# Kernel tuning notes

Measured on AMD Instinct MI355X. Metric: run time of the kernel, lower is better.

## Reference

```python
import jax, jax.numpy as jnp
import numpy as np

# e2m1 FP4 value table: sign bit in nibble MSB, values {0,0.5,1,1.5,2,3,4,6}
_E2M1 = jnp.array([0.0, 0.5, 1.0, 1.5, 2.0, 3.0, 4.0, 6.0,
                   -0.0, -0.5, -1.0, -1.5, -2.0, -3.0, -4.0, -6.0], dtype=jnp.float32)


def _dequant_fp4(packed, scales, group_size):
    """packed: [E, out, in//8] uint32; scales: [E, in//group_size, out] -> [E, out, in] f32."""
    shifts = jnp.arange(8, dtype=jnp.uint32) * 4  # nibble shift amounts 0,4,...,28
    nib = (packed[..., None] >> shifts) & jnp.uint32(0xF)  # [E, out, in//8, 8]
    E, O, P, _ = nib.shape
    nib = nib.reshape(E, O, P * 8).astype(jnp.int32)
    w = _E2M1[nib]  # [E, out, in] f32
    gids = jnp.arange(P * 8) // group_size  # group id per input column
    sc = jnp.transpose(scales, (0, 2, 1))[:, :, gids]  # [E, out, in]
    return w * sc


def setup_inputs() -> dict:
    E, H, I, T, K, G = 8, 2048, 1408, 2048, 2, 128
    key = jax.random.key(0)
    ks = jax.random.split(key, 9)
    x = jax.random.normal(ks[0], (T, H), dtype=jnp.float32)
    gate_packed = jax.random.bits(ks[1], (E, I, H // 8), dtype=jnp.uint32)
    up_packed = jax.random.bits(ks[2], (E, I, H // 8), dtype=jnp.uint32)
    down_packed = jax.random.bits(ks[3], (E, H, I // 8), dtype=jnp.uint32)
    gate_scales = jax.random.uniform(ks[4], (E, H // G, I), jnp.float32, 0.5, 1.5)
    up_scales = jax.random.uniform(ks[5], (E, H // G, I), jnp.float32, 0.5, 1.5)
    down_scales = jax.random.uniform(ks[6], (E, I // G, H), jnp.float32, 0.5, 1.5)
    topk_idx = jax.random.randint(ks[7], (T, K), 0, E, dtype=jnp.int32)
    w = jax.random.uniform(ks[8], (T, K), jnp.float32)
    topk_w = w / jnp.sum(w, axis=-1, keepdims=True)
    return {"x": x,
            "gate_packed": gate_packed, "gate_scales": gate_scales,
            "up_packed": up_packed, "up_scales": up_scales,
            "down_packed": down_packed, "down_scales": down_scales,
            "topk_idx": topk_idx, "topk_w": topk_w, "group_size": G}


def reference(x, gate_packed, gate_scales, up_packed, up_scales,
              down_packed, down_scales, topk_idx, topk_w, group_size):
    # Fused dequant (nibble unpack + e2m1 table + per-group scale) for all experts
    gate_w = _dequant_fp4(gate_packed, gate_scales, group_size)  # [E, I, H]
    up_w = _dequant_fp4(up_packed, up_scales, group_size)        # [E, I, H]
    down_w = _dequant_fp4(down_packed, down_scales, group_size)  # [E, H, I]
    # Grouped SwiGLU expert MLP (dense over E=8 experts, gather routed outputs)
    g = jnp.einsum('th,eih->eti', x, gate_w)
    u = jnp.einsum('th,eih->eti', x, up_w)
    h = jax.nn.silu(g) * u                                        # [E, T, I]
    y = jnp.einsum('eti,ehi->eth', h, down_w)                     # [E, T, H]
    T = x.shape[0]
    sel = y[topk_idx, jnp.arange(T)[:, None], :]                  # [T, K, H]
    return jnp.sum(sel * topk_w[..., None], axis=1)               # [T, H]
```

## Files before the change

### kernel.cpp

```cpp
#include <hip/hip_runtime.h>
#include <hip/hip_bf16.h>
#include <stdint.h>

#define E_ 8
#define H_ 2048
#define I_ 1408
#define T_ 2048
#define K_ 2
#define G_ 128

typedef __bf16 bf16;
typedef bf16 bf16x8 __attribute__((ext_vector_type(8)));
typedef float f32x4 __attribute__((ext_vector_type(4)));

__device__ __forceinline__ uint32_t prm(uint32_t hi, uint32_t lo, uint32_t sel) {
    return __builtin_amdgcn_perm(hi, lo, sel);
}

struct DequantTab { uint32_t thi0, thi1, tlo0, tlo1; };

__device__ __forceinline__ DequantTab build_tab(float s) {
    union { bf16 h[8]; uint32_t u[4]; } tb;
    tb.h[0] = (bf16)(0.0f);
    tb.h[1] = (bf16)(0.5f * s);
    tb.h[2] = (bf16)(1.0f * s);
    tb.h[3] = (bf16)(1.5f * s);
    tb.h[4] = (bf16)(2.0f * s);
    tb.h[5] = (bf16)(3.0f * s);
    tb.h[6] = (bf16)(4.0f * s);
    tb.h[7] = (bf16)(6.0f * s);
    DequantTab t;
    t.thi0 = prm(tb.u[1], tb.u[0], 0x07050301u);
    t.tlo0 = prm(tb.u[1], tb.u[0], 0x06040200u);
    t.thi1 = prm(tb.u[3], tb.u[2], 0x07050301u);
    t.tlo1 = prm(tb.u[3], tb.u[2], 0x06040200u);
    return t;
}

__device__ __forceinline__ uint4 dequant8t(uint32_t p, const DequantTab& t) {
    const uint32_t pr = p >> 4;
    const uint32_t pe = p  & 0x07070707u;
    const uint32_t po = pr & 0x07070707u;
    const uint32_t He = prm(t.thi1, t.thi0, pe) | ((p  & 0x08080808u) << 4);
    const uint32_t Le = prm(t.tlo1, t.tlo0, pe);
    const uint32_t Ho = prm(t.thi1, t.thi0, po) | ((pr & 0x08080808u) << 4);
    const uint32_t Lo = prm(t.tlo1, t.tlo0, po);
    const uint32_t E01 = prm(He, Le, 0x05010400u);
    const uint32_t E23 = prm(He, Le, 0x07030602u);
    const uint32_t O01 = prm(Ho, Lo, 0x05010400u);
    const uint32_t O23 = prm(Ho, Lo, 0x07030602u);
    return make_uint4(prm(O01, E01, 0x05040100u),
                      prm(O01, E01, 0x07060302u),
                      prm(O23, E23, 0x05040100u),
                      prm(O23, E23, 0x07060302u));
}

__device__ __forceinline__ void gld16(void* lds, const void* g) {
    __builtin_amdgcn_global_load_lds(
        (__attribute__((address_space(1))) void*)g,
        (__attribute__((address_space(3))) void*)lds, 16, 0, 0);
}

#define SB0() __builtin_amdgcn_sched_barrier(0)

#define DQW(WD, PW, TAB) do { \
    uint4 d0_ = dequant8t((PW).x, (TAB)); \
    uint4 d1_ = dequant8t((PW).y, (TAB)); \
    uint4 d2_ = dequant8t((PW).z, (TAB)); \
    uint4 d3_ = dequant8t((PW).w, (TAB)); \
    *(uint4*)&WD[wrow][((cb + 0) ^ rs) * 8] = d0_; \
    *(uint4*)&WD[wrow][((cb + 1) ^ rs) * 8] = d1_; \
    *(uint4*)&WD[wrow][((cb + 2) ^ rs) * 8] = d2_; \
    *(uint4*)&WD[wrow][((cb + 3) ^ rs) * 8] = d3_; \
} while (0)

__global__ void route_count(const int* __restrict__ topk_idx, int* __restrict__ counts) {
    int p = blockIdx.x * blockDim.x + threadIdx.x;
    if (p < T_ * K_) atomicAdd(&counts[topk_idx[p]], 1);
}

__global__ void route_scan(const int* __restrict__ counts, int* __restrict__ offsets,
                           int* __restrict__ tmap) {
    if (threadIdx.x == 0) {
        int acc = 0, ti = 0;
        for (int e = 0; e < E_; e++) {
            offsets[e] = acc;
            int nt = (counts[e] + 127) >> 7;
            for (int j = 0; j < nt; j++) tmap[ti++] = (e << 16) | j;
            acc += counts[e];
        }
        offsets[E_] = acc;
        for (; ti < 64; ti++) tmap[ti] = -1;
    }
}

__global__ void route_fill(const int* __restrict__ topk_idx, const float* __restrict__ topk_w,
                           int* __restrict__ cursors, const int* __restrict__ offsets,
                           int* __restrict__ tok, float* __restrict__ wgt,
                           int* __restrict__ inv) {
    int p = blockIdx.x * blockDim.x + threadIdx.x;
    if (p < T_ * K_) {
        int e = topk_idx[p];
        int slot = atomicAdd(&cursors[e], 1);
        int idx = offsets[e] + slot;
        tok[idx] = p / K_;
        wgt[idx] = topk_w[p];
        inv[p] = idx;
    }
}

__global__ __launch_bounds__(256)
void xcast_kernel(const float* __restrict__ x, uint4* __restrict__ xb) {
    const int i = blockIdx.x * 256 + threadIdx.x;
    const float4 a = ((const float4*)x)[i * 2];
    const float4 b = ((const float4*)x)[i * 2 + 1];
    union { uint4 u; bf16 h[8]; } r;
    r.h[0] = (bf16)a.x; r.h[1] = (bf16)a.y; r.h[2] = (bf16)a.z; r.h[3] = (bf16)a.w;
    r.h[4] = (bf16)b.x; r.h[5] = (bf16)b.y; r.h[6] = (bf16)b.z; r.h[7] = (bf16)b.w;
    xb[i] = r.u;
}

__global__ __launch_bounds__(256, 2)
void gemm1t_kernel(const bf16* __restrict__ xb,
                   const uint32_t* __restrict__ gate_packed,
                   const float* __restrict__ gate_scales,
                   const uint32_t* __restrict__ up_packed,
                   const float* __restrict__ up_scales,
                   const int* __restrict__ offsets,
                   const int* __restrict__ tmap,
                   const int* __restrict__ tok, bf16* __restrict__ h_buf)
{
    const int tm = tmap[blockIdx.x];
    if (tm < 0) return;
    const int e = tm >> 16, ty = tm & 0xffff;
    const int row0 = offsets[e];
    const int cnt = offsets[e + 1] - row0;
    const int itile = blockIdx.y;

    __shared__ __align__(16) bf16 xs0[128][64];
    __shared__ __align__(16) bf16 xs1[128][64];
    __shared__ __align__(16) bf16 wgs0[64][64];
    __shared__ __align__(16) bf16 wgs1[64][64];
    __shared__ __align__(16) bf16 wus0[64][64];
    __shared__ __align__(16) bf16 wus1[64][64];

    const int tid = threadIdx.x;

    const int xr = tid >> 3;
    const int xc = tid & 7;
    const int xch = (xc ^ (xr & 7)) * 8;
    const bf16* xsrc[4];
    bf16 *xdst0[4], *xdst1[4];
#pragma unroll
    for (int j = 0; j < 4; ++j) {
        int g = ty * 128 + xr + j * 32;
        g = (g < cnt) ? g : (cnt - 1);
        xsrc[j] = xb + (size_t)tok[row0 + g] * H_ + xch;
        xdst0[j] = &xs0[xr + j * 32][xc * 8];
        xdst1[j] = &xs1[xr + j * 32][xc * 8];
    }

    const int mat  = tid >> 7;
    const int id   = tid & 127;
    const int wrow = id >> 1;
    const int quad = id & 1;
    const int cb = quad * 4, rs = wrow & 7;
    const int irow = itile * 64 + wrow;
    const uint32_t* wp_row = (mat ? up_packed : gate_packed)
        + (size_t)e * I_ * (H_ / 8) + (size_t)irow * (H_ / 8) + quad * 4;
    const float* ws_row = (mat ? up_scales : gate_scales)
        + (size_t)e * (H_ / G_) * I_ + irow;
    bf16 (* const wd0)[64] = mat ? wus0 : wgs0;
    bf16 (* const wd1)[64] = mat ? wus1 : wgs1;

    const int wave = tid >> 6, lane = tid & 63;
    const int wy = wave >> 1, wx = wave & 1;
    const int lrow = lane & 15, kq = lane >> 4;

    f32x4 accg[4][2] = {};
    f32x4 accu[4][2] = {};

    constexpr int NG = H_ / G_;

#define MFMA1(XS, WG, WU) do { \
    _Pragma("unroll") \
    for (int kh = 0; kh < 2; ++kh) { \
        bf16x8 a[4], bg[2], bu[2]; \
        _Pragma("unroll") \
        for (int mi = 0; mi < 4; ++mi) { \
            const int ra = wy * 64 + mi * 16 + lrow; \
            a[mi] = *(const bf16x8*)&XS[ra][((kh * 4 + kq) ^ (ra & 7)) * 8]; \
        } \
        _Pragma("unroll") \
        for (int ni = 0; ni < 2; ++ni) { \
            const int rbq = wx * 32 + ni * 16 + lrow; \
            const int cbq = ((kh * 4 + kq) ^ (rbq & 7)) * 8; \
            bg[ni] = *(const bf16x8*)&WG[rbq][cbq]; \
            bu[ni] = *(const bf16x8*)&WU[rbq][cbq]; \
        } \
        _Pragma("unroll") \
        for (int mi = 0; mi < 4; ++mi) \
            _Pragma("unroll") \
            for (int ni = 0; ni < 2; ++ni) { \
                accg[mi][ni] = __builtin_amdgcn_mfma_f32_16x16x32_bf16(a[mi], bg[ni], accg[mi][ni], 0, 0, 0); \
                accu[mi][ni] = __builtin_amdgcn_mfma_f32_16x16x32_bf16(a[mi], bu[ni], accu[mi][ni], 0, 0, 0); \
            } \
    } \
} while (0)

#pragma unroll
    for (int j = 0; j < 4; ++j) gld16(xdst0[j], xsrc[j]);
    SB0();
    uint4 pw0 = *(const uint4*)(wp_row);
    uint4 pwO = *(const uint4*)(wp_row + 8);
    float sc0 = ws_row[0];
    SB0();
    DequantTab tab = build_tab(sc0);
    DQW(wd0, pw0, tab);
    asm volatile("s_waitcnt lgkmcnt(0)" ::: "memory");
    __builtin_amdgcn_s_barrier();
    SB0();

    float scn = 0.f;
    uint4 pwE;
    for (int kg = 0; kg < NG; ++kg) {
        const bool last = (kg == NG - 1);
#pragma unroll
        for (int j = 0; j < 4; ++j) gld16(xdst1[j], xsrc[j] + (kg * 2 + 1) * 64);
        SB0();
        if (!last) {
            pwE = *(const uint4*)(wp_row + (size_t)(kg * 2 + 2) * 8);
            scn = ws_row[(size_t)(kg + 1) * I_];
        }
        SB0();
        DQW(wd1, pwO, tab);
        MFMA1(xs0, wgs0, wus0);
        SB0();
        if (!last) asm volatile("s_waitcnt vmcnt(2) lgkmcnt(0)" ::: "memory");
        else       asm volatile("s_waitcnt vmcnt(0) lgkmcnt(0)" ::: "memory");
        __builtin_amdgcn_s_barrier();
        SB0();

        if (!last) {
#pragma unroll
            for (int j = 0; j < 4; ++j) gld16(xdst0[j], xsrc[j] + (kg * 2 + 2) * 64);
            SB0();
            pwO = *(const uint4*)(wp_row + (size_t)(kg * 2 + 3) * 8);
            SB0();
            tab = build_tab(scn);
            DQW(wd0, pwE, tab);
            MFMA1(xs1, wgs1, wus1);
            SB0();
            asm volatile("s_waitcnt vmcnt(1) lgkmcnt(0)" ::: "memory");
            __builtin_amdgcn_s_barrier();
            SB0();
        } else {
            MFMA1(xs1, wgs1, wus1);
            SB0();
            asm volatile("s_waitcnt lgkmcnt(0)" ::: "memory");
            __builtin_amdgcn_s_barrier();
            SB0();
        }
    }

#pragma unroll
    for (int mi = 0; mi < 4; ++mi)
#pragma unroll
        for (int ni = 0; ni < 2; ++ni) {
            const int icol = itile * 64 + wx * 32 + ni * 16 + lrow;
#pragma unroll
            for (int r = 0; r < 4; ++r) {
                const int grow = ty * 128 + wy * 64 + mi * 16 + kq * 4 + r;
                if (grow < cnt) {
                    const float gv = accg[mi][ni][r];
                    const float hv = gv / (1.f + __expf(-gv)) * accu[mi][ni][r];
                    h_buf[(size_t)(row0 + grow) * I_ + icol] = (bf16)hv;
                }
            }
        }
#undef MFMA1
}

__global__ __launch_bounds__(256, 2)
void gemm2t_kernel(const bf16* __restrict__ h_buf,
                   const uint32_t* __restrict__ down_packed,
                   const float* __restrict__ down_scales,
                   const int* __restrict__ offsets,
                   const int* __restrict__ tmap,
                   const float* __restrict__ wgt, float* __restrict__ yp)
{
    const int tm = tmap[blockIdx.x];
    if (tm < 0) return;
    const int e = tm >> 16, ty = tm & 0xffff;
    const int row0 = offsets[e];
    const int cnt = offsets[e + 1] - row0;
    const int htile = blockIdx.y;

    __shared__ __align__(16) bf16 hs0[128][64];
    __shared__ __align__(16) bf16 hs1[128][64];
    __shared__ __align__(16) bf16 wds0[128][64];
    __shared__ __align__(16) bf16 wds1[128][64];

    const int tid = threadIdx.x;

    const int xr = tid >> 3;
    const int xc = tid & 7;
    const int xch = (xc ^ (xr & 7)) * 8;
    const bf16* hsrc[4];
    bf16 *hdst0[4], *hdst1[4];
#pragma unroll
    for (int j = 0; j < 4; ++j) {
        int g = ty * 128 + xr + j * 32;
        g = (g < cnt) ? g : (cnt - 1);
        hsrc[j] = h_buf + (size_t)(row0 + g) * I_ + xch;
        hdst0[j] = &hs0[xr + j * 32][xc * 8];
        hdst1[j] = &hs1[xr + j * 32][xc * 8];
    }

    const int wrow = tid >> 1;
    const int quad = tid & 1;
    const int cb = quad * 4, rs = wrow & 7;
    const int hrow = htile * 128 + wrow;
    const uint32_t* dp_row = down_packed + (size_t)e * H_ * (I_ / 8) + (size_t)hrow * (I_ / 8) + quad * 4;
    const float* ds_row = down_scales + (size_t)e * (I_ / G_) * H_ + hrow;

    const int wave = tid >> 6, lane = tid & 63;
    const int wy = wave >> 1, wx = wave & 1;
    const int lrow = lane & 15, kq = lane >> 4;

    f32x4 acc[4][4] = {};

    constexpr int NG = I_ / G_;

#define MFMA2(HS, WD) do { \
    _Pragma("unroll") \
    for (int kh = 0; kh < 2; ++kh) { \
        bf16x8 a[4], b[4]; \
        _Pragma("unroll") \
        for (int mi = 0; mi < 4; ++mi) { \
            const int ra = wy * 64 + mi * 16 + lrow; \
            a[mi] = *(const bf16x8*)&HS[ra][((kh * 4 + kq) ^ (ra & 7)) * 8]; \
        } \
        _Pragma("unroll") \
        for (int ni = 0; ni < 4; ++ni) { \
            const int rbq = wx * 64 + ni * 16 + lrow; \
            b[ni] = *(const bf16x8*)&WD[rbq][((kh * 4 + kq) ^ (rbq & 7)) * 8]; \
        } \
        _Pragma("unroll") \
        for (int mi = 0; mi < 4; ++mi) \
            _Pragma("unroll") \
            for (int ni = 0; ni < 4; ++ni) \
                acc[mi][ni] = __builtin_amdgcn_mfma_f32_16x16x32_bf16(a[mi], b[ni], acc[mi][ni], 0, 0, 0); \
    } \
} while (0)

#pragma unroll
    for (int j = 0; j < 4; ++j) gld16(hdst0[j], hsrc[j]);
    SB0();
    uint4 pw0 = *(const uint4*)(dp_row);
    uint4 pwO = *(const uint4*)(dp_row + 8);
    float sc0 = ds_row[0];
    SB0();
    DequantTab tab = build_tab(sc0);
    DQW(wds0, pw0, tab);
    asm volatile("s_waitcnt lgkmcnt(0)" ::: "memory");
    __builtin_amdgcn_s_barrier();
    SB0();

    float scn = 0.f;
    uint4 pwE;
    for (int kg = 0; kg < NG; ++kg) {
        const bool last = (kg == NG - 1);
#pragma unroll
        for (int j = 0; j < 4; ++j) gld16(hdst1[j], hsrc[j] + (kg * 2 + 1) * 64);
        SB0();
        if (!last) {
            pwE = *(const uint4*)(dp_row + (size_t)(kg * 2 + 2) * 8);
            scn = ds_row[(size_t)(kg + 1) * H_];
        }
        SB0();
        DQW(wds1, pwO, tab);
        MFMA2(hs0, wds0);
        SB0();
        if (!last) asm volatile("s_waitcnt vmcnt(2) lgkmcnt(0)" ::: "memory");
        else       asm volatile("s_waitcnt vmcnt(0) lgkmcnt(0)" ::: "memory");
        __builtin_amdgcn_s_barrier();
        SB0();

        if (!last) {
#pragma unroll
            for (int j = 0; j < 4; ++j) gld16(hdst0[j], hsrc[j] + (kg * 2 + 2) * 64);
            SB0();
            pwO = *(const uint4*)(dp_row + (size_t)(kg * 2 + 3) * 8);
            SB0();
            tab = build_tab(scn);
            DQW(wds0, pwE, tab);
            MFMA2(hs1, wds1);
            SB0();
            asm volatile("s_waitcnt vmcnt(1) lgkmcnt(0)" ::: "memory");
            __builtin_amdgcn_s_barrier();
            SB0();
        } else {
            MFMA2(hs1, wds1);
            SB0();
            asm volatile("s_waitcnt lgkmcnt(0)" ::: "memory");
            __builtin_amdgcn_s_barrier();
            SB0();
        }
    }

#pragma unroll
    for (int mi = 0; mi < 4; ++mi)
#pragma unroll
        for (int r = 0; r < 4; ++r) {
            const int lr = wy * 64 + mi * 16 + kq * 4 + r;
            const int grow = ty * 128 + lr;
            if (grow < cnt) {
                const float w = wgt[row0 + grow];
#pragma unroll
                for (int ni = 0; ni < 4; ++ni) {
                    const int col = htile * 128 + wx * 64 + ni * 16 + lrow;
                    yp[(size_t)(row0 + grow) * H_ + col] = acc[mi][ni][r] * w;
                }
            }
        }
#undef MFMA2
}

__global__ __launch_bounds__(256)
void combine_kernel(const float* __restrict__ yp, const int* __restrict__ inv,
                    float* __restrict__ out) {
    const int idx = blockIdx.x * 256 + threadIdx.x;
    const int t = idx >> 9;
    const int c = idx & 511;
    const float4 a = ((const float4*)yp)[(size_t)inv[t * 2] * (H_ / 4) + c];
    const float4 b = ((const float4*)yp)[(size_t)inv[t * 2 + 1] * (H_ / 4) + c];
    float4 o;
    o.x = a.x + b.x; o.y = a.y + b.y; o.z = a.z + b.z; o.w = a.w + b.w;
    ((float4*)out)[idx] = o;
}

extern "C" void kernel_launch(void* const* d_in, const int* in_sizes, int n_in,
                              void* d_out, int out_size, void* d_ws, size_t ws_size,
                              hipStream_t stream) {
    const float* x = (const float*)d_in[0];
    const uint32_t* gate_packed = (const uint32_t*)d_in[1];
    const float* gate_scales = (const float*)d_in[2];
    const uint32_t* up_packed = (const uint32_t*)d_in[3];
    const float* up_scales = (const float*)d_in[4];
    const uint32_t* down_packed = (const uint32_t*)d_in[5];
    const float* down_scales = (const float*)d_in[6];
    const int* topk_idx = (const int*)d_in[7];
    const float* topk_w = (const float*)d_in[8];
    float* out = (float*)d_out;

    char* ws = (char*)d_ws;
    int* counts  = (int*)ws;
    int* cursors = (int*)(ws + 32);
    int* offsets = (int*)(ws + 64);
    int* tmap    = (int*)(ws + 128);
    int* tok     = (int*)(ws + 640);
    float* wgt   = (float*)(ws + 17024);
    int* inv     = (int*)(ws + 33408);
    bf16* h_buf  = (bf16*)(ws + 49792);
    bf16* xb     = (bf16*)(ws + 49792 + 11534336ull);
    float* yp    = (float*)(ws + 49792 + 11534336ull + 8388608ull);

    hipMemsetAsync(d_ws, 0, 1024, stream);

    route_count<<<(T_ * K_ + 255) / 256, 256, 0, stream>>>(topk_idx, counts);
    route_scan<<<1, 64, 0, stream>>>(counts, offsets, tmap);
    route_fill<<<(T_ * K_ + 255) / 256, 256, 0, stream>>>(topk_idx, topk_w, cursors, offsets,
                                                          tok, wgt, inv);
    xcast_kernel<<<T_ * H_ / 8 / 256, 256, 0, stream>>>(x, (uint4*)xb);

    dim3 g1(40, I_ / 64);
    gemm1t_kernel<<<g1, 256, 0, stream>>>(xb, gate_packed, gate_scales, up_packed, up_scales,
                                          offsets, tmap, tok, h_buf);
    dim3 g2(40, H_ / 128);
    gemm2t_kernel<<<g2, 256, 0, stream>>>(h_buf, down_packed, down_scales,
                                          offsets, tmap, wgt, yp);
    combine_kernel<<<T_ * H_ / 4 / 256, 256, 0, stream>>>(yp, inv, out);
}
```

Measured before the change: 273.4 us.

## Stage packed FP4 weights in LDS and dequantize at fragment load

Both expert GEMM kernels now copy the raw packed FP4 words into a small padded LDS buffer instead of dequantized bf16 tiles. Each MFMA fragment is then dequantized in registers right before use, with per-row scale tables built once per group. The weight prefetch is also made deeper, with a three-stage register pipeline and retuned waitcnts. The aim is to cut LDS footprint and LDS write and read traffic, which may raise occupancy. In exchange, dequant work is duplicated across waves that share a weight column, adds register pressure, and puts VALU work next to the MFMAs.

```diff
diff --git a/kernel.cpp b/kernel.cpp
--- a/kernel.cpp
+++ b/kernel.cpp
@@ -55,6 +55,12 @@
                       prm(O23, E23, 0x07060302u));
 }
 
+__device__ __forceinline__ bf16x8 dq_frag(uint32_t p, const DequantTab& t) {
+    union { uint4 u; bf16x8 v; } r;
+    r.u = dequant8t(p, t);
+    return r.v;
+}
+
 __device__ __forceinline__ void gld16(void* lds, const void* g) {
     __builtin_amdgcn_global_load_lds(
         (__attribute__((address_space(1))) void*)g,
@@ -62,17 +68,6 @@
 }
 
 #define SB0() __builtin_amdgcn_sched_barrier(0)
-
-#define DQW(WD, PW, TAB) do { \
-    uint4 d0_ = dequant8t((PW).x, (TAB)); \
-    uint4 d1_ = dequant8t((PW).y, (TAB)); \
-    uint4 d2_ = dequant8t((PW).z, (TAB)); \
-    uint4 d3_ = dequant8t((PW).w, (TAB)); \
-    *(uint4*)&WD[wrow][((cb + 0) ^ rs) * 8] = d0_; \
-    *(uint4*)&WD[wrow][((cb + 1) ^ rs) * 8] = d1_; \
-    *(uint4*)&WD[wrow][((cb + 2) ^ rs) * 8] = d2_; \
-    *(uint4*)&WD[wrow][((cb + 3) ^ rs) * 8] = d3_; \
-} while (0)
 
 __global__ void route_count(const int* __restrict__ topk_idx, int* __restrict__ counts) {
     int p = blockIdx.x * blockDim.x + threadIdx.x;
@@ -139,10 +134,7 @@
 
     __shared__ __align__(16) bf16 xs0[128][64];
     __shared__ __align__(16) bf16 xs1[128][64];
-    __shared__ __align__(16) bf16 wgs0[64][64];
-    __shared__ __align__(16) bf16 wgs1[64][64];
-    __shared__ __align__(16) bf16 wus0[64][64];
-    __shared__ __align__(16) bf16 wus1[64][64];
+    __shared__ __align__(16) uint32_t wraw[2][2][64][12];
 
     const int tid = threadIdx.x;
 
@@ -164,25 +156,26 @@
     const int id   = tid & 127;
     const int wrow = id >> 1;
     const int quad = id & 1;
-    const int cb = quad * 4, rs = wrow & 7;
     const int irow = itile * 64 + wrow;
     const uint32_t* wp_row = (mat ? up_packed : gate_packed)
         + (size_t)e * I_ * (H_ / 8) + (size_t)irow * (H_ / 8) + quad * 4;
-    const float* ws_row = (mat ? up_scales : gate_scales)
-        + (size_t)e * (H_ / G_) * I_ + irow;
-    bf16 (* const wd0)[64] = mat ? wus0 : wgs0;
-    bf16 (* const wd1)[64] = mat ? wus1 : wgs1;
 
     const int wave = tid >> 6, lane = tid & 63;
     const int wy = wave >> 1, wx = wave & 1;
     const int lrow = lane & 15, kq = lane >> 4;
 
+    const float* gsc = gate_scales + (size_t)e * (H_ / G_) * I_;
+    const float* usc = up_scales + (size_t)e * (H_ / G_) * I_;
+    const int rb0 = itile * 64 + wx * 32 + lrow;
+    const int rbr0 = wx * 32 + lrow;
+
     f32x4 accg[4][2] = {};
     f32x4 accu[4][2] = {};
 
     constexpr int NG = H_ / G_;
-
-#define MFMA1(XS, WG, WU) do { \
+    constexpr int NT = 2 * NG;
+
+#define MFMA1(XS, WB) do { \
     _Pragma("unroll") \
     for (int kh = 0; kh < 2; ++kh) { \
         bf16x8 a[4], bg[2], bu[2]; \
@@ -192,18 +185,16 @@
             a[mi] = *(const bf16x8*)&XS[ra][((kh * 4 + kq) ^ (ra & 7)) * 8]; \
         } \
         _Pragma("unroll") \
-        for (int ni = 0; ni < 2; ++ni) { \
-            const int rbq = wx * 32 + ni * 16 + lrow; \
-            const int cbq = ((kh * 4 + kq) ^ (rbq & 7)) * 8; \
-            bg[ni] = *(const bf16x8*)&WG[rbq][cbq]; \
-            bu[ni] = *(const bf16x8*)&WU[rbq][cbq]; \
+        for (int n = 0; n < 2; ++n) { \
+            bg[n] = dq_frag(wraw[WB][0][rbr0 + n * 16][kh * 4 + kq], tab[0][n]); \
+            bu[n] = dq_frag(wraw[WB][1][rbr0 + n * 16][kh * 4 + kq], tab[1][n]); \
         } \
         _Pragma("unroll") \
         for (int mi = 0; mi < 4; ++mi) \
             _Pragma("unroll") \
-            for (int ni = 0; ni < 2; ++ni) { \
-                accg[mi][ni] = __builtin_amdgcn_mfma_f32_16x16x32_bf16(a[mi], bg[ni], accg[mi][ni], 0, 0, 0); \
-                accu[mi][ni] = __builtin_amdgcn_mfma_f32_16x16x32_bf16(a[mi], bu[ni], accu[mi][ni], 0, 0, 0); \
+            for (int n = 0; n < 2; ++n) { \
+                accg[mi][n] = __builtin_amdgcn_mfma_f32_16x16x32_bf16(a[mi], bg[n], accg[mi][n], 0, 0, 0); \
+                accu[mi][n] = __builtin_amdgcn_mfma_f32_16x16x32_bf16(a[mi], bu[n], accu[mi][n], 0, 0, 0); \
             } \
     } \
 } while (0)
@@ -212,68 +203,79 @@
     for (int j = 0; j < 4; ++j) gld16(xdst0[j], xsrc[j]);
     SB0();
     uint4 pw0 = *(const uint4*)(wp_row);
-    uint4 pwO = *(const uint4*)(wp_row + 8);
-    float sc0 = ws_row[0];
-    SB0();
-    DequantTab tab = build_tab(sc0);
-    DQW(wd0, pw0, tab);
-    asm volatile("s_waitcnt lgkmcnt(0)" ::: "memory");
+    uint4 pwA = *(const uint4*)(wp_row + 8);
+    uint4 pwB = *(const uint4*)(wp_row + 16);
+    float sc[2][2], scn[2][2];
+    sc[0][0] = gsc[rb0]; sc[0][1] = gsc[rb0 + 16];
+    sc[1][0] = usc[rb0]; sc[1][1] = usc[rb0 + 16];
+    SB0();
+    *(uint4*)&wraw[0][mat][wrow][quad * 4] = pw0;
+    asm volatile("s_waitcnt vmcnt(0) lgkmcnt(0)" ::: "memory");
     __builtin_amdgcn_s_barrier();
     SB0();
 
-    float scn = 0.f;
-    uint4 pwE;
+    uint4 pwN;
     for (int kg = 0; kg < NG; ++kg) {
         const bool last = (kg == NG - 1);
+        DequantTab tab[2][2];
+#pragma unroll
+        for (int m = 0; m < 2; ++m)
+#pragma unroll
+            for (int n = 0; n < 2; ++n)
+                tab[m][n] = build_tab(sc[m][n]);
+
+        *(uint4*)&wraw[1][mat][wrow][quad * 4] = pwA;
+        SB0();
 #pragma unroll
         for (int j = 0; j < 4; ++j) gld16(xdst1[j], xsrc[j] + (kg * 2 + 1) * 64);
         SB0();
+        { int tl = kg * 2 + 3; if (tl > NT - 1) tl = NT - 1;
+          pwN = *(const uint4*)(wp_row + (size_t)tl * 8); }
+        { const int kgn = last ? kg : kg + 1;
+          scn[0][0] = gsc[(size_t)kgn * I_ + rb0]; scn[0][1] = gsc[(size_t)kgn * I_ + rb0 + 16];
+          scn[1][0] = usc[(size_t)kgn * I_ + rb0]; scn[1][1] = usc[(size_t)kgn * I_ + rb0 + 16]; }
+        SB0();
+        MFMA1(xs0, 0);
+        SB0();
+        asm volatile("s_waitcnt vmcnt(5) lgkmcnt(0)" ::: "memory");
+        __builtin_amdgcn_s_barrier();
+        SB0();
+        pwA = pwB; pwB = pwN;
+
         if (!last) {
-            pwE = *(const uint4*)(wp_row + (size_t)(kg * 2 + 2) * 8);
-            scn = ws_row[(size_t)(kg + 1) * I_];
+            *(uint4*)&wraw[0][mat][wrow][quad * 4] = pwA;
+            SB0();
+#pragma unroll
+            for (int j = 0; j < 4; ++j) gld16(xdst0[j], xsrc[j] + (kg * 2 + 2) * 64);
+            SB0();
+            { int tl = kg * 2 + 4; if (tl > NT - 1) tl = NT - 1;
+              pwN = *(const uint4*)(wp_row + (size_t)tl * 8); }
+            SB0();
         }
-        SB0();
-        DQW(wd1, pwO, tab);
-        MFMA1(xs0, wgs0, wus0);
-        SB0();
-        if (!last) asm volatile("s_waitcnt vmcnt(2) lgkmcnt(0)" ::: "memory");
+        MFMA1(xs1, 1);
+        SB0();
+        if (!last) asm volatile("s_waitcnt vmcnt(1) lgkmcnt(0)" ::: "memory");
         else       asm volatile("s_waitcnt vmcnt(0) lgkmcnt(0)" ::: "memory");
         __builtin_amdgcn_s_barrier();
         SB0();
-
-        if (!last) {
-#pragma unroll
-            for (int j = 0; j < 4; ++j) gld16(xdst0[j], xsrc[j] + (kg * 2 + 2) * 64);
-            SB0();
-            pwO = *(const uint4*)(wp_row + (size_t)(kg * 2 + 3) * 8);
-            SB0();
-            tab = build_tab(scn);
-            DQW(wd0, pwE, tab);
-            MFMA1(xs1, wgs1, wus1);
-            SB0();
-            asm volatile("s_waitcnt vmcnt(1) lgkmcnt(0)" ::: "memory");
-            __builtin_amdgcn_s_barrier();
-            SB0();
-        } else {
-            MFMA1(xs1, wgs1, wus1);
-            SB0();
-            asm volatile("s_waitcnt lgkmcnt(0)" ::: "memory");
-            __builtin_amdgcn_s_barrier();
-            SB0();
-        }
+        if (!last) { pwA = pwB; pwB = pwN; }
+#pragma unroll
+        for (int m = 0; m < 2; ++m)
+#pragma unroll
+            for (int n = 0; n < 2; ++n) sc[m][n] = scn[m][n];
     }
 
 #pragma unroll
     for (int mi = 0; mi < 4; ++mi)
 #pragma unroll
-        for (int ni = 0; ni < 2; ++ni) {
-            const int icol = itile * 64 + wx * 32 + ni * 16 + lrow;
+        for (int n = 0; n < 2; ++n) {
+            const int icol = itile * 64 + wx * 32 + n * 16 + lrow;
 #pragma unroll
             for (int r = 0; r < 4; ++r) {
                 const int grow = ty * 128 + wy * 64 + mi * 16 + kq * 4 + r;
                 if (grow < cnt) {
-                    const float gv = accg[mi][ni][r];
-                    const float hv = gv / (1.f + __expf(-gv)) * accu[mi][ni][r];
+                    const float gv = accg[mi][n][r];
+                    const float hv = gv / (1.f + __expf(-gv)) * accu[mi][n][r];
                     h_buf[(size_t)(row0 + grow) * I_ + icol] = (bf16)hv;
                 }
             }
@@ -298,8 +300,7 @@
 
     __shared__ __align__(16) bf16 hs0[128][64];
     __shared__ __align__(16) bf16 hs1[128][64];
-    __shared__ __align__(16) bf16 wds0[128][64];
-    __shared__ __align__(16) bf16 wds1[128][64];
+    __shared__ __align__(16) uint32_t wraw[2][128][12];
 
     const int tid = threadIdx.x;
 
@@ -319,20 +320,23 @@
 
     const int wrow = tid >> 1;
     const int quad = tid & 1;
-    const int cb = quad * 4, rs = wrow & 7;
     const int hrow = htile * 128 + wrow;
     const uint32_t* dp_row = down_packed + (size_t)e * H_ * (I_ / 8) + (size_t)hrow * (I_ / 8) + quad * 4;
-    const float* ds_row = down_scales + (size_t)e * (I_ / G_) * H_ + hrow;
 
     const int wave = tid >> 6, lane = tid & 63;
     const int wy = wave >> 1, wx = wave & 1;
     const int lrow = lane & 15, kq = lane >> 4;
 
+    const float* dsc = down_scales + (size_t)e * (I_ / G_) * H_;
+    const int rb0 = htile * 128 + wx * 64 + lrow;
+    const int rbr0 = wx * 64 + lrow;
+
     f32x4 acc[4][4] = {};
 
     constexpr int NG = I_ / G_;
-
-#define MFMA2(HS, WD) do { \
+    constexpr int NT = 2 * NG;
+
+#define MFMA2(HS, WB) do { \
     _Pragma("unroll") \
     for (int kh = 0; kh < 2; ++kh) { \
         bf16x8 a[4], b[4]; \
@@ -342,15 +346,13 @@
             a[mi] = *(const bf16x8*)&HS[ra][((kh * 4 + kq) ^ (ra & 7)) * 8]; \
         } \
         _Pragma("unroll") \
-        for (int ni = 0; ni < 4; ++ni) { \
-            const int rbq = wx * 64 + ni * 16 + lrow; \
-            b[ni] = *(const bf16x8*)&WD[rbq][((kh * 4 + kq) ^ (rbq & 7)) * 8]; \
-        } \
+        for (int n = 0; n < 4; ++n) \
+            b[n] = dq_frag(wraw[WB][rbr0 + n * 16][kh * 4 + kq], tab[n]); \
         _Pragma("unroll") \
         for (int mi = 0; mi < 4; ++mi) \
             _Pragma("unroll") \
-            for (int ni = 0; ni < 4; ++ni) \
-                acc[mi][ni] = __builtin_amdgcn_mfma_f32_16x16x32_bf16(a[mi], b[ni], acc[mi][ni], 0, 0, 0); \
+            for (int n = 0; n < 4; ++n) \
+                acc[mi][n] = __builtin_amdgcn_mfma_f32_16x16x32_bf16(a[mi], b[n], acc[mi][n], 0, 0, 0); \
     } \
 } while (0)
 
@@ -358,69 +360,73 @@
     for (int j = 0; j < 4; ++j) gld16(hdst0[j], hsrc[j]);
     SB0();
     uint4 pw0 = *(const uint4*)(dp_row);
-    uint4 pwO = *(const uint4*)(dp_row + 8);
-    float sc0 = ds_row[0];
-    SB0();
-    DequantTab tab = build_tab(sc0);
-    DQW(wds0, pw0, tab);
-    asm volatile("s_waitcnt lgkmcnt(0)" ::: "memory");
+    uint4 pwA = *(const uint4*)(dp_row + 8);
+    uint4 pwB = *(const uint4*)(dp_row + 16);
+    float sc[4], scn[4];
+    sc[0] = dsc[rb0]; sc[1] = dsc[rb0 + 16]; sc[2] = dsc[rb0 + 32]; sc[3] = dsc[rb0 + 48];
+    SB0();
+    *(uint4*)&wraw[0][wrow][quad * 4] = pw0;
+    asm volatile("s_waitcnt vmcnt(0) lgkmcnt(0)" ::: "memory");
     __builtin_amdgcn_s_barrier();
     SB0();
 
-    float scn = 0.f;
-    uint4 pwE;
+    uint4 pwN;
     for (int kg = 0; kg < NG; ++kg) {
         const bool last = (kg == NG - 1);
+        DequantTab tab[4];
+#pragma unroll
+        for (int n = 0; n < 4; ++n) tab[n] = build_tab(sc[n]);
+
+        *(uint4*)&wraw[1][wrow][quad * 4] = pwA;
+        SB0();
 #pragma unroll
         for (int j = 0; j < 4; ++j) gld16(hdst1[j], hsrc[j] + (kg * 2 + 1) * 64);
         SB0();
+        { int tl = kg * 2 + 3; if (tl > NT - 1) tl = NT - 1;
+          pwN = *(const uint4*)(dp_row + (size_t)tl * 8); }
+        { const int kgn = last ? kg : kg + 1;
+          scn[0] = dsc[(size_t)kgn * H_ + rb0];      scn[1] = dsc[(size_t)kgn * H_ + rb0 + 16];
+          scn[2] = dsc[(size_t)kgn * H_ + rb0 + 32]; scn[3] = dsc[(size_t)kgn * H_ + rb0 + 48]; }
+        SB0();
+        MFMA2(hs0, 0);
+        SB0();
+        asm volatile("s_waitcnt vmcnt(5) lgkmcnt(0)" ::: "memory");
+        __builtin_amdgcn_s_barrier();
+        SB0();
+        pwA = pwB; pwB = pwN;
+
         if (!last) {
-            pwE = *(const uint4*)(dp_row + (size_t)(kg * 2 + 2) * 8);
-            scn = ds_row[(size_t)(kg + 1) * H_];
+            *(uint4*)&wraw[0][wrow][quad * 4] = pwA;
+            SB0();
+#pragma unroll
+            for (int j = 0; j < 4; ++j) gld16(hdst0[j], hsrc[j] + (kg * 2 + 2) * 64);
+            SB0();
+            { int tl = kg * 2 + 4; if (tl > NT - 1) tl = NT - 1;
+              pwN = *(const uint4*)(dp_row + (size_t)tl * 8); }
+            SB0();
         }
-        SB0();
-        DQW(wds1, pwO, tab);
-        MFMA2(hs0, wds0);
-        SB0();
-        if (!last) asm volatile("s_waitcnt vmcnt(2) lgkmcnt(0)" ::: "memory");
+        MFMA2(hs1, 1);
+        SB0();
+        if (!last) asm volatile("s_waitcnt vmcnt(1) lgkmcnt(0)" ::: "memory");
         else       asm volatile("s_waitcnt vmcnt(0) lgkmcnt(0)" ::: "memory");
         __builtin_amdgcn_s_barrier();
         SB0();
-
-        if (!last) {
-#pragma unroll
-            for (int j = 0; j < 4; ++j) gld16(hdst0[j], hsrc[j] + (kg * 2 + 2) * 64);
-            SB0();
-            pwO = *(const uint4*)(dp_row + (size_t)(kg * 2 + 3) * 8);
-            SB0();
-            tab = build_tab(scn);
-            DQW(wds0, pwE, tab);
-            MFMA2(hs1, wds1);
-            SB0();
-            asm volatile("s_waitcnt vmcnt(1) lgkmcnt(0)" ::: "memory");
-            __builtin_amdgcn_s_barrier();
-            SB0();
-        } else {
-            MFMA2(hs1, wds1);
-            SB0();
-            asm volatile("s_waitcnt lgkmcnt(0)" ::: "memory");
-            __builtin_amdgcn_s_barrier();
-            SB0();
-        }
+        if (!last) { pwA = pwB; pwB = pwN; }
+#pragma unroll
+        for (int n = 0; n < 4; ++n) sc[n] = scn[n];
     }
 
 #pragma unroll
     for (int mi = 0; mi < 4; ++mi)
 #pragma unroll
         for (int r = 0; r < 4; ++r) {
-            const int lr = wy * 64 + mi * 16 + kq * 4 + r;
-            const int grow = ty * 128 + lr;
+            const int grow = ty * 128 + wy * 64 + mi * 16 + kq * 4 + r;
             if (grow < cnt) {
                 const float w = wgt[row0 + grow];
 #pragma unroll
-                for (int ni = 0; ni < 4; ++ni) {
-                    const int col = htile * 128 + wx * 64 + ni * 16 + lrow;
-                    yp[(size_t)(row0 + grow) * H_ + col] = acc[mi][ni][r] * w;
+                for (int n = 0; n < 4; ++n) {
+                    const int col = htile * 128 + wx * 64 + n * 16 + lrow;
+                    yp[(size_t)(row0 + grow) * H_ + col] = acc[mi][n][r] * w;
                 }
             }
         }
```

Result: slower. 296.2 us (+8.3%).
